# Performance work log

Hardware: AMD Instinct MI355X
Metric: run time of the kernel (lower is better)

## Reference

```python
import jax, jax.numpy as jnp
import numpy as np

N = 20000      # nodes
E = 640000     # edges
FIN = 128
FQK = 128
FV = 128
H = 8
FH = FQK // H   # 16
FHV = FV // H   # 16
FTOT = 2 * FQK + FV


def setup_inputs() -> dict:
    key = jax.random.key(0)
    kx, kw, ks, kd, kb = jax.random.split(key, 5)
    x = jax.random.normal(kx, (N, FIN), dtype=jnp.float32)
    # nn.Linear(Fin, Ftot, bias=False): weight [Ftot, Fin]
    W = jax.random.normal(kw, (FTOT, FIN), dtype=jnp.float32) / np.sqrt(FIN)
    # src must be sorted (scatter ops assume grouped-by-src, size src[-1]+1)
    src = jnp.sort(jax.random.randint(ks, (E,), 0, N, dtype=jnp.int64))
    src = src.at[-1].set(N - 1)  # ensure full output size N
    dest = jax.random.randint(kd, (E,), 0, N, dtype=jnp.int64)
    ei = jnp.stack([src, dest])
    batch = jnp.sort(jax.random.randint(kb, (N,), 0, 16, dtype=jnp.int64))
    return {"x": x, "W": W, "batch": batch, "ei": ei}


def reference(x, W, batch, ei):
    src, dest = ei[0], ei[1]
    scaling = float(FH) ** (-0.5)
    proj = x @ W.T                                  # [N, Ftot]
    q, k, v = jnp.split(proj, [FQK, 2 * FQK], axis=-1)
    q = (q * scaling).reshape(-1, H, FH)            # [N, H, Fh]
    k = k.reshape(-1, H, FH)
    v = v.reshape(-1, H, FHV)
    qs, ks, vs = q[src], k[dest], v[dest]           # [E, H, Fh] gathers
    aw = jnp.einsum('ehf,ehf->eh', qs, ks)          # per-edge dot products
    # scatter_softmax: global (not per-segment) max subtraction, as in source
    xm = aw.max(axis=0)                              # [H]
    exp = jnp.exp(aw - xm) + 1e-8                    # [E, H]
    expsum = jax.ops.segment_sum(exp, src, num_segments=N)[src]
    attn = exp / expsum                              # [E, H]
    out = jax.ops.segment_sum(attn[:, :, None] * vs, src, num_segments=N)
    return out.reshape(-1, H * FHV)                  # [N, Fv]
```

## Files before the change

### kernel.cpp

```cpp
#include <hip/hip_runtime.h>

constexpr int FIN = 128;

constexpr float XM0 = 8.0f;

typedef __attribute__((ext_vector_type(8))) short bf8x;
typedef __attribute__((ext_vector_type(8))) unsigned short u16x8;
typedef __attribute__((ext_vector_type(4))) float f4x;

__device__ inline unsigned short f2bf(float v) {
  unsigned int u = __float_as_uint(v);
  unsigned int r = u + 0x7FFFu + ((u >> 16) & 1u);
  return (unsigned short)(r >> 16);
}
__device__ inline float bf2f(unsigned short s) {
  return __uint_as_float(((unsigned int)s) << 16);
}

__global__ __launch_bounds__(256, 2) void proj_kernel(
    const float* __restrict__ x, const float* __restrict__ W,
    float* __restrict__ qbuf, unsigned short* __restrict__ kv, int N) {
  __shared__ unsigned short xhi[128][72], xlo[128][72];
  __shared__ unsigned short whi[128][72], wlo[128][72];

  const int tid = threadIdx.x;
  const int r0 = blockIdx.y * 128;
  const int c0 = blockIdx.x * 128;
  const int lane = tid & 63;
  const int w = tid >> 6;
  const int mbase = (w >> 1) * 64;
  const int nbase = (w & 1) * 64;
  const int lr = lane & 15;
  const int q4 = lane >> 4;

  f4x acc[4][4];
#pragma unroll
  for (int mt = 0; mt < 4; ++mt)
#pragma unroll
    for (int nt = 0; nt < 4; ++nt)
#pragma unroll
      for (int k = 0; k < 4; ++k) acc[mt][nt][k] = 0.f;

  for (int p = 0; p < 2; ++p) {
    if (p) __syncthreads();
#pragma unroll
    for (int pass = 0; pass < 8; ++pass) {
      const int idx = tid + pass * 256;
      const int kq = idx & 15, r = idx >> 4;
      float4 xv = make_float4(0.f, 0.f, 0.f, 0.f);
      if (r0 + r < N) xv = *(const float4*)(x + (size_t)(r0 + r) * FIN + p * 64 + kq * 4);
      const float4 wv = *(const float4*)(W + (size_t)(c0 + r) * FIN + p * 64 + kq * 4);
      const float xa[4] = {xv.x, xv.y, xv.z, xv.w};
      const float wa[4] = {wv.x, wv.y, wv.z, wv.w};
      unsigned short xh[4], xl[4], wh[4], wl[4];
#pragma unroll
      for (int i = 0; i < 4; ++i) {
        xh[i] = f2bf(xa[i]); xl[i] = f2bf(xa[i] - bf2f(xh[i]));
        wh[i] = f2bf(wa[i]); wl[i] = f2bf(wa[i] - bf2f(wh[i]));
      }
      *(ushort4*)&xhi[r][kq * 4] = make_ushort4(xh[0], xh[1], xh[2], xh[3]);
      *(ushort4*)&xlo[r][kq * 4] = make_ushort4(xl[0], xl[1], xl[2], xl[3]);
      *(ushort4*)&whi[r][kq * 4] = make_ushort4(wh[0], wh[1], wh[2], wh[3]);
      *(ushort4*)&wlo[r][kq * 4] = make_ushort4(wl[0], wl[1], wl[2], wl[3]);
    }
    __syncthreads();

#pragma unroll
    for (int kit = 0; kit < 2; ++kit) {
      const int ko = kit * 32 + q4 * 8;
      bf8x ah[4], al[4], bh[4], bl[4];
#pragma unroll
      for (int i2 = 0; i2 < 4; ++i2) {
        ah[i2] = *(const bf8x*)&xhi[mbase + i2 * 16 + lr][ko];
        al[i2] = *(const bf8x*)&xlo[mbase + i2 * 16 + lr][ko];
        bh[i2] = *(const bf8x*)&whi[nbase + i2 * 16 + lr][ko];
        bl[i2] = *(const bf8x*)&wlo[nbase + i2 * 16 + lr][ko];
      }
#pragma unroll
      for (int mt = 0; mt < 4; ++mt)
#pragma unroll
        for (int nt = 0; nt < 4; ++nt) {
          acc[mt][nt] = __builtin_amdgcn_mfma_f32_16x16x32_bf16(ah[mt], bh[nt], acc[mt][nt], 0, 0, 0);
          acc[mt][nt] = __builtin_amdgcn_mfma_f32_16x16x32_bf16(ah[mt], bl[nt], acc[mt][nt], 0, 0, 0);
          acc[mt][nt] = __builtin_amdgcn_mfma_f32_16x16x32_bf16(al[mt], bh[nt], acc[mt][nt], 0, 0, 0);
        }
    }
  }

#pragma unroll
  for (int mt = 0; mt < 4; ++mt)
#pragma unroll
    for (int nt = 0; nt < 4; ++nt)
#pragma unroll
      for (int rr = 0; rr < 4; ++rr) {
        const int row = r0 + mbase + mt * 16 + q4 * 4 + rr;
        if (row < N) {
          const int c = c0 + nbase + nt * 16 + lr;
          const float v = acc[mt][nt][rr];
          if (c < 128) qbuf[(size_t)row * 128 + c] = v * 0.25f;
          else kv[(size_t)row * 256 + (c - 128)] = f2bf(v);
        }
      }
}

__global__ void rowptr_kernel(const int* __restrict__ src,
                              int* __restrict__ row_ptr, int N, int E) {
  const int n = blockIdx.x * blockDim.x + threadIdx.x;
  if (n <= N) {
    int lo = 0, hi = E;
    while (lo < hi) {
      int mid = (lo + hi) >> 1;
      if (src[mid] < n) lo = mid + 1; else hi = mid;
    }
    row_ptr[n] = lo;
  }
}

__global__ __launch_bounds__(128, 8) void attn_kernel(
    const float* __restrict__ qbuf, const unsigned short* __restrict__ kv,
    const int* __restrict__ dest, const int* __restrict__ row_ptr,
    float* __restrict__ out) {
  __shared__ unsigned short ks[32][136];
  __shared__ unsigned short vs[32][136];
  __shared__ float attn_t[8][36];
  __shared__ int dst_s[32];
  __shared__ float red_es[8][8];
  __shared__ float es_tot[8];
  float(*red_acc)[8] = (float(*)[8]) & ks[0][0];

  const int n = blockIdx.x;
  const int t = threadIdx.x;
  const int e0 = row_ptr[n], e1 = row_ptr[n + 1];

  const int hd = t & 7, sd = t >> 3;
  const int oc = t & 15, sa = t >> 4;
  const int ha = oc >> 1;
  const int srow = t >> 2, sseg = t & 3;

  float q[16];
  {
    const float* qp = qbuf + (size_t)n * 128 + hd * 16;
#pragma unroll
    for (int j4 = 0; j4 < 4; ++j4) {
      const float4 qv = *(const float4*)(qp + j4 * 4);
      q[j4 * 4 + 0] = qv.x; q[j4 * 4 + 1] = qv.y;
      q[j4 * 4 + 2] = qv.z; q[j4 * 4 + 3] = qv.w;
    }
  }

  float acc8[8];
#pragma unroll
  for (int j = 0; j < 8; ++j) acc8[j] = 0.f;
  float es_a = 0.f;

  for (int ce = e0; ce < e1; ce += 32) {
    const int m = (e1 - ce < 32) ? (e1 - ce) : 32;
    if (t < m) dst_s[t] = dest[ce + t];
    __syncthreads();
    if (srow < m) {
      const unsigned short* base = kv + (size_t)dst_s[srow] * 256;
#pragma unroll
      for (int pp = 0; pp < 4; ++pp) {
        const int seg = sseg + pp * 4;
        const u16x8 kk = *(const u16x8*)(base + seg * 8);
        const u16x8 vv = *(const u16x8*)(base + 128 + seg * 8);
        *(u16x8*)&ks[srow][seg * 8] = kk;
        *(u16x8*)&vs[srow][seg * 8] = vv;
      }
    }
    __syncthreads();
#pragma unroll
    for (int rep = 0; rep < 2; ++rep) {
      const int e = sd + rep * 16;
      if (e < m) {
        float s = 0.f;
#pragma unroll
        for (int j2 = 0; j2 < 2; ++j2) {
          const u16x8 kk = *(const u16x8*)&ks[e][hd * 16 + j2 * 8];
#pragma unroll
          for (int jj = 0; jj < 8; ++jj) s += q[j2 * 8 + jj] * bf2f(kk[jj]);
        }
        attn_t[hd][e] = __expf(s - XM0) + 1e-8f;
      }
    }
    __syncthreads();
#pragma unroll
    for (int g = 0; g < 4; ++g) {
      const int i = sa + g * 8;
      if (i < m) {
        const float a = attn_t[ha][i];
        es_a += a;
        const u16x8 vv = *(const u16x8*)&vs[i][oc * 8];
#pragma unroll
        for (int jj = 0; jj < 8; ++jj) acc8[jj] += a * bf2f(vv[jj]);
      }
    }
  }

  *(float4*)&red_acc[t][0] = make_float4(acc8[0], acc8[1], acc8[2], acc8[3]);
  *(float4*)&red_acc[t][4] = make_float4(acc8[4], acc8[5], acc8[6], acc8[7]);
  if (!(oc & 1)) red_es[sa][ha] = es_a;
  __syncthreads();
  if (t < 8) {
    float s = 0.f;
#pragma unroll
    for (int ss = 0; ss < 8; ++ss) s += red_es[ss][t];
    es_tot[t] = s;
  }
  __syncthreads();
  const int fo = t >> 3, fj = t & 7, fh = t >> 4;
  float a = 0.f;
#pragma unroll
  for (int ss = 0; ss < 8; ++ss) a += red_acc[fo + 16 * ss][fj];
  out[(size_t)n * 128 + t] = (e1 > e0) ? (a / es_tot[fh]) : 0.f;
}

extern "C" void kernel_launch(void* const* d_in, const int* in_sizes, int n_in,
                              void* d_out, int out_size, void* d_ws, size_t ws_size,
                              hipStream_t stream) {
  const float* x = (const float*)d_in[0];
  const float* W = (const float*)d_in[1];
  const int* ei = (const int*)d_in[3];

  const int N = in_sizes[0] / FIN;
  const int E = in_sizes[3] / 2;
  const int* src = ei;
  const int* dst = ei + E;
  float* out = (float*)d_out;

  char* ws = (char*)d_ws;
  float* qbuf = (float*)ws;
  size_t off = (size_t)N * 128 * sizeof(float);
  unsigned short* kvb = (unsigned short*)(ws + off);
  off += (size_t)N * 256 * sizeof(unsigned short);
  int* row_ptr = (int*)(ws + off);

  dim3 pgrid(3, (N + 127) / 128);
  proj_kernel<<<pgrid, 256, 0, stream>>>(x, W, qbuf, kvb, N);
  rowptr_kernel<<<(N + 1 + 255) / 256, 256, 0, stream>>>(src, row_ptr, N, E);
  attn_kernel<<<N, 128, 0, stream>>>(qbuf, kvb, dst, row_ptr, out);
}
```

Measured before the change: 134.2 us.

## Fuse row_ptr search into projection and load K/V directly into registers

The row_ptr binary search moves into the projection kernel, which removes a separate launch. The attention kernel stops staging gathered K/V rows through shared memory. Each thread now loads the K and V fragments it needs straight from global memory into registers, which drops the LDS copy and one barrier per 32-edge chunk. Launch bounds drop from 8 to 4 blocks per SM to leave room for the extra registers, which may reduce occupancy and latency hiding for the gathers.

```diff
diff --git a/kernel.cpp b/kernel.cpp
--- a/kernel.cpp
+++ b/kernel.cpp
@@ -19,13 +19,27 @@
 
 __global__ __launch_bounds__(256, 2) void proj_kernel(
     const float* __restrict__ x, const float* __restrict__ W,
-    float* __restrict__ qbuf, unsigned short* __restrict__ kv, int N) {
+    float* __restrict__ qbuf, unsigned short* __restrict__ kv, int N,
+    const int* __restrict__ src, int* __restrict__ row_ptr, int E) {
   __shared__ unsigned short xhi[128][72], xlo[128][72];
   __shared__ unsigned short whi[128][72], wlo[128][72];
 
   const int tid = threadIdx.x;
   const int r0 = blockIdx.y * 128;
   const int c0 = blockIdx.x * 128;
+
+  {
+    const int gid = (blockIdx.y * gridDim.x + blockIdx.x) * 256 + tid;
+    if (gid <= N) {
+      int lo = 0, hi = E;
+      while (lo < hi) {
+        int mid = (lo + hi) >> 1;
+        if (src[mid] < gid) lo = mid + 1; else hi = mid;
+      }
+      row_ptr[gid] = lo;
+    }
+  }
+
   const int lane = tid & 63;
   const int w = tid >> 6;
   const int mbase = (w >> 1) * 64;
@@ -103,30 +117,15 @@
       }
 }
 
-__global__ void rowptr_kernel(const int* __restrict__ src,
-                              int* __restrict__ row_ptr, int N, int E) {
-  const int n = blockIdx.x * blockDim.x + threadIdx.x;
-  if (n <= N) {
-    int lo = 0, hi = E;
-    while (lo < hi) {
-      int mid = (lo + hi) >> 1;
-      if (src[mid] < n) lo = mid + 1; else hi = mid;
-    }
-    row_ptr[n] = lo;
-  }
-}
-
-__global__ __launch_bounds__(128, 8) void attn_kernel(
+__global__ __launch_bounds__(128, 4) void attn_kernel(
     const float* __restrict__ qbuf, const unsigned short* __restrict__ kv,
     const int* __restrict__ dest, const int* __restrict__ row_ptr,
     float* __restrict__ out) {
-  __shared__ unsigned short ks[32][136];
-  __shared__ unsigned short vs[32][136];
+  __shared__ int dst_s[32];
   __shared__ float attn_t[8][36];
-  __shared__ int dst_s[32];
+  __shared__ float red_acc[128][8];
   __shared__ float red_es[8][8];
   __shared__ float es_tot[8];
-  float(*red_acc)[8] = (float(*)[8]) & ks[0][0];
 
   const int n = blockIdx.x;
   const int t = threadIdx.x;
@@ -135,7 +134,6 @@
   const int hd = t & 7, sd = t >> 3;
   const int oc = t & 15, sa = t >> 4;
   const int ha = oc >> 1;
-  const int srow = t >> 2, sseg = t & 3;
 
   float q[16];
   {
@@ -155,44 +153,49 @@
 
   for (int ce = e0; ce < e1; ce += 32) {
     const int m = (e1 - ce < 32) ? (e1 - ce) : 32;
-    if (t < m) dst_s[t] = dest[ce + t];
+    if (t < 32 && ce + t < e1) dst_s[t] = dest[ce + t];
     __syncthreads();
-    if (srow < m) {
-      const unsigned short* base = kv + (size_t)dst_s[srow] * 256;
-#pragma unroll
-      for (int pp = 0; pp < 4; ++pp) {
-        const int seg = sseg + pp * 4;
-        const u16x8 kk = *(const u16x8*)(base + seg * 8);
-        const u16x8 vv = *(const u16x8*)(base + 128 + seg * 8);
-        *(u16x8*)&ks[srow][seg * 8] = kk;
-        *(u16x8*)&vs[srow][seg * 8] = vv;
-      }
-    }
-    __syncthreads();
+
+    u16x8 kf[2][2];
+    u16x8 vf[4];
+#pragma unroll
+    for (int rep = 0; rep < 2; ++rep) {
+      const int e = sd + rep * 16;
+      if (e < m) {
+        const unsigned short* kb = kv + (size_t)dst_s[e] * 256 + hd * 16;
+        kf[rep][0] = *(const u16x8*)kb;
+        kf[rep][1] = *(const u16x8*)(kb + 8);
+      }
+    }
+#pragma unroll
+    for (int g = 0; g < 4; ++g) {
+      const int i = sa + g * 8;
+      if (i < m)
+        vf[g] = *(const u16x8*)(kv + (size_t)dst_s[i] * 256 + 128 + oc * 8);
+    }
+
 #pragma unroll
     for (int rep = 0; rep < 2; ++rep) {
       const int e = sd + rep * 16;
       if (e < m) {
         float s = 0.f;
 #pragma unroll
-        for (int j2 = 0; j2 < 2; ++j2) {
-          const u16x8 kk = *(const u16x8*)&ks[e][hd * 16 + j2 * 8];
-#pragma unroll
-          for (int jj = 0; jj < 8; ++jj) s += q[j2 * 8 + jj] * bf2f(kk[jj]);
-        }
+        for (int jj = 0; jj < 8; ++jj) s += q[jj] * bf2f(kf[rep][0][jj]);
+#pragma unroll
+        for (int jj = 0; jj < 8; ++jj) s += q[8 + jj] * bf2f(kf[rep][1][jj]);
         attn_t[hd][e] = __expf(s - XM0) + 1e-8f;
       }
     }
     __syncthreads();
+
 #pragma unroll
     for (int g = 0; g < 4; ++g) {
       const int i = sa + g * 8;
       if (i < m) {
         const float a = attn_t[ha][i];
         es_a += a;
-        const u16x8 vv = *(const u16x8*)&vs[i][oc * 8];
-#pragma unroll
-        for (int jj = 0; jj < 8; ++jj) acc8[jj] += a * bf2f(vv[jj]);
+#pragma unroll
+        for (int jj = 0; jj < 8; ++jj) acc8[jj] += a * bf2f(vf[g][jj]);
       }
     }
   }
@@ -236,7 +239,6 @@
   int* row_ptr = (int*)(ws + off);
 
   dim3 pgrid(3, (N + 127) / 128);
-  proj_kernel<<<pgrid, 256, 0, stream>>>(x, W, qbuf, kvb, N);
-  rowptr_kernel<<<(N + 1 + 255) / 256, 256, 0, stream>>>(src, row_ptr, N, E);
+  proj_kernel<<<pgrid, 256, 0, stream>>>(x, W, qbuf, kvb, N, src, row_ptr, E);
   attn_kernel<<<N, 128, 0, stream>>>(qbuf, kvb, dst, row_ptr, out);
 }
```

Result: no change. 132.0 us (-1.6%).
